# Optimization experiments

Hardware: AMD Instinct MI355X
Metric: run time of the kernel (lower is better)

Reference implementation:

```python
import jax, jax.numpy as jnp
import numpy as np

B, C_IN, N, E, C_OUT = 1, 128, 50000, 800000, 128
NEG_SLOPE = 0.3


def setup_inputs() -> dict:
    key = jax.random.key(0)
    k1, k2, k3, k4, k5 = jax.random.split(key, 5)
    in_features = jax.random.normal(k1, (B, C_IN, N), dtype=jnp.float32)
    weight = jax.random.normal(k2, (C_OUT, 2 * C_IN), dtype=jnp.float32) / np.sqrt(2 * C_IN)
    bias = jax.random.normal(k3, (C_OUT,), dtype=jnp.float32) * 0.01
    reduce_index = jax.random.randint(k4, (E,), 0, N, dtype=jnp.int64)
    gather_index = jax.random.randint(k5, (E,), 0, N, dtype=jnp.int64)
    return {"in_features": in_features, "weight": weight, "bias": bias,
            "reduce_index": reduce_index, "gather_index": gather_index}


def reference(in_features, weight, bias, reduce_index, gather_index):
    n_vertices = in_features.shape[-1]
    # gather endpoint features: [B, C, E]
    vertices = in_features[..., reduce_index]
    neighbors = in_features[..., gather_index]
    # concat [x_i, x_j - x_i] -> [B, 2C, E]
    concat = jnp.concatenate([vertices, neighbors - vertices], axis=1)
    # 1x1 Conv1d == per-edge matmul: [B, O, E]
    f_e = jnp.einsum('oc,bce->boe', weight, concat) + bias[None, :, None]
    # scatter-mean over reduce_index (include_self=False: empty segments stay 0)
    f_e_efirst = jnp.moveaxis(f_e, -1, 0)                      # [E, B, O]
    sums = jax.ops.segment_sum(f_e_efirst, reduce_index, num_segments=n_vertices)  # [N,B,O]
    counts = jax.ops.segment_sum(jnp.ones((reduce_index.shape[0],), dtype=f_e.dtype),
                                 reduce_index, num_segments=n_vertices)            # [N]
    mean = sums / jnp.maximum(counts, 1.0)[:, None, None]
    out = jnp.moveaxis(mean, 0, -1)                            # [B, O, N]
    # LeakyReLU(0.3)
    return jnp.where(out >= 0, out, NEG_SLOPE * out)
```

## Files before the change

### kernel.cpp

```cpp
#include <hip/hip_runtime.h>
#include <stddef.h>

#define CCH 128
#define CAP 64
#define FILL_CS 4096

typedef unsigned int  uint;
typedef unsigned short ushort;
typedef unsigned char uchar;
typedef short bf16x8 __attribute__((ext_vector_type(8)));
typedef float f32x4  __attribute__((ext_vector_type(4)));
typedef float f32x2  __attribute__((ext_vector_type(2)));

__device__ __forceinline__ ushort f2bf(float f) {
    uint b = __float_as_uint(f);
    b += 0x7FFFu + ((b >> 16) & 1u);
    return (ushort)(b >> 16);
}
__device__ __forceinline__ float bflo(uint u) { return __uint_as_float(u << 16); }
__device__ __forceinline__ float bfhi(uint u) { return __uint_as_float(u & 0xFFFF0000u); }

__global__ void prep_zero(const float* __restrict__ w, ushort* __restrict__ wstb,
                          int* __restrict__ zero_buf, int NZ) {
    int i = blockIdx.x * 256 + threadIdx.x;
    if (i < CCH * 256) {
        int c = i & 255;
        float v = w[i];
        if (c < 128) v -= w[i + 128];
        wstb[i] = f2bf(v);
    }
    for (int n = i; n < NZ; n += gridDim.x * 256) zero_buf[n] = 0;
}

__global__ __launch_bounds__(256) void transpose_fill(
        const float* __restrict__ x, ushort* __restrict__ xtb,
        uchar* __restrict__ xtf8,
        const int* __restrict__ ridx, const int* __restrict__ gidx,
        int* __restrict__ counts, int* __restrict__ bucket,
        int N, int E, int psz, int T, int F) {
    __shared__ float tile[CCH][33];
    int b = blockIdx.x;
    int mtf = (T < F) ? T : F;
    int twice = 2 * mtf;
    bool is_t; int sub;
    if (b < twice) { is_t = !(b & 1); sub = b >> 1; }
    else           { is_t = (T > F);  sub = (b - twice) + mtf; }
    int tid = threadIdx.x;

    if (is_t) {
        int n0 = sub * 32;
        {
            int tx = tid & 31, r = tid >> 5;
            int n = n0 + tx;
            #pragma unroll
            for (int k = 0; k < 16; ++k) {
                int c = k * 8 + r;
                tile[c][tx] = (n < N) ? x[(size_t)c * N + n] : 0.f;
            }
        }
        __syncthreads();
        #pragma unroll
        for (int p = 0; p < 2; ++p) {
            int nn = p * 16 + (tid >> 4);
            int c8 = (tid & 15) * 8;
            if (n0 + nn < N) {
                float f[8];
                #pragma unroll
                for (int j = 0; j < 8; ++j) f[j] = tile[c8 + j][nn];
                uint4 v;
                v.x = (uint)f2bf(f[0]) | ((uint)f2bf(f[1]) << 16);
                v.y = (uint)f2bf(f[2]) | ((uint)f2bf(f[3]) << 16);
                v.z = (uint)f2bf(f[4]) | ((uint)f2bf(f[5]) << 16);
                v.w = (uint)f2bf(f[6]) | ((uint)f2bf(f[7]) << 16);
                *(uint4*)(xtb + (size_t)(n0 + nn) * CCH + c8) = v;
                int p0 = __builtin_amdgcn_cvt_pk_fp8_f32(f[0], f[1], 0, false);
                p0     = __builtin_amdgcn_cvt_pk_fp8_f32(f[2], f[3], p0, true);
                int p1 = __builtin_amdgcn_cvt_pk_fp8_f32(f[4], f[5], 0, false);
                p1     = __builtin_amdgcn_cvt_pk_fp8_f32(f[6], f[7], p1, true);
                uint2 w8; w8.x = (uint)p0; w8.y = (uint)p1;
                *(uint2*)(xtf8 + (size_t)(n0 + nn) * CCH + c8) = w8;
            }
        }
    } else {
        int part  = sub & 7;
        int chunk = sub >> 3;
        int e0 = chunk * FILL_CS;
        int e1 = e0 + FILL_CS; if (e1 > E) e1 = E;
        for (int base = e0; base < e1; base += 1024) {
            int rr[4], gg[4];
            bool act[4];
            #pragma unroll
            for (int q = 0; q < 4; ++q) {
                int e = base + q * 256 + tid;
                bool in = (e < e1);
                int ec = in ? e : e0;
                rr[q] = ridx[ec];
                gg[q] = gidx[ec];
                act[q] = in && (rr[q] / psz == part);
            }
            #pragma unroll
            for (int q = 0; q < 4; ++q) {
                if (act[q]) {
                    int p = atomicAdd(&counts[rr[q]], 1);
                    if (p < CAP) bucket[rr[q] * CAP + p] = gg[q];
                }
            }
        }
    }
}

__global__ __launch_bounds__(256) void gather_mean(
        const uint*  __restrict__ xtf8u,
        const int*   __restrict__ counts,
        const int*   __restrict__ bucket,
        ushort*      __restrict__ gmb,
        int N) {
    int wave = threadIdx.x >> 6;
    int l = threadIdx.x & 63;
    int lq = l & 31;
    int half = l >> 5;
    #pragma unroll
    for (int i = 0; i < 2; ++i) {
        int n = blockIdx.x * 8 + wave * 2 + i;
        if (n >= N) return;
        int deg = __builtin_amdgcn_readfirstlane(counts[n]);
        int dg  = (deg < CAP) ? deg : CAP;
        const int* row = bucket + n * CAP;
        float4 acc = make_float4(0.f, 0.f, 0.f, 0.f);
        int k = 0;
        for (; k + 16 <= dg; k += 16) {
            uint u[8];
            #pragma unroll
            for (int q = 0; q < 8; ++q) {
                int g = row[k + 2 * q + half];
                u[q] = xtf8u[(size_t)g * 32 + lq];
            }
            #pragma unroll
            for (int q = 0; q < 8; ++q) {
                f32x2 a = __builtin_amdgcn_cvt_pk_f32_fp8(u[q], false);
                f32x2 b = __builtin_amdgcn_cvt_pk_f32_fp8(u[q], true);
                acc.x += a.x; acc.y += a.y; acc.z += b.x; acc.w += b.y;
            }
        }
        for (; k + 8 <= dg; k += 8) {
            uint u[4];
            #pragma unroll
            for (int q = 0; q < 4; ++q) {
                int g = row[k + 2 * q + half];
                u[q] = xtf8u[(size_t)g * 32 + lq];
            }
            #pragma unroll
            for (int q = 0; q < 4; ++q) {
                f32x2 a = __builtin_amdgcn_cvt_pk_f32_fp8(u[q], false);
                f32x2 b = __builtin_amdgcn_cvt_pk_f32_fp8(u[q], true);
                acc.x += a.x; acc.y += a.y; acc.z += b.x; acc.w += b.y;
            }
        }
        for (; k + 2 <= dg; k += 2) {
            int g = row[k + half];
            uint u = xtf8u[(size_t)g * 32 + lq];
            f32x2 a = __builtin_amdgcn_cvt_pk_f32_fp8(u, false);
            f32x2 b = __builtin_amdgcn_cvt_pk_f32_fp8(u, true);
            acc.x += a.x; acc.y += a.y; acc.z += b.x; acc.w += b.y;
        }
        if (k < dg && half == 0) {
            int g = row[k];
            uint u = xtf8u[(size_t)g * 32 + lq];
            f32x2 a = __builtin_amdgcn_cvt_pk_f32_fp8(u, false);
            f32x2 b = __builtin_amdgcn_cvt_pk_f32_fp8(u, true);
            acc.x += a.x; acc.y += a.y; acc.z += b.x; acc.w += b.y;
        }
        acc.x += __shfl_xor(acc.x, 32);
        acc.y += __shfl_xor(acc.y, 32);
        acc.z += __shfl_xor(acc.z, 32);
        acc.w += __shfl_xor(acc.w, 32);
        float inv = (deg > 0) ? 1.f / (float)deg : 0.f;
        if (half == 0) {
            ushort4 r;
            r.x = f2bf(acc.x * inv);
            r.y = f2bf(acc.y * inv);
            r.z = f2bf(acc.z * inv);
            r.w = f2bf(acc.w * inv);
            *(ushort4*)(gmb + (size_t)n * CCH + lq * 4) = r;
        }
    }
}

__global__ __launch_bounds__(256) void gemm_mfma(
        const ushort* __restrict__ wstb,
        const ushort* __restrict__ xtb,
        const ushort* __restrict__ gmb,
        const int*    __restrict__ counts,
        const float*  __restrict__ bias,
        float* __restrict__ out,
        int N) {
    int t = threadIdx.x;
    int wv = t >> 6;
    int l  = t & 63;
    int l15 = l & 15;
    int lk  = l >> 4;
    int n = blockIdx.x * 64 + wv * 16 + l15;
    int nc = (n < N) ? n : (N - 1);

    f32x4 acc[8];
    #pragma unroll
    for (int mf = 0; mf < 8; ++mf) acc[mf] = (f32x4){0.f, 0.f, 0.f, 0.f};

    const ushort* brow_x = xtb + (size_t)nc * CCH + lk * 8;
    const ushort* brow_g = gmb + (size_t)nc * CCH + lk * 8;
    const ushort* arow   = wstb + (size_t)l15 * 256 + lk * 8;

    #pragma unroll
    for (int ks = 0; ks < 8; ++ks) {
        const ushort* bp = (ks < 4) ? (brow_x + ks * 32) : (brow_g + (ks - 4) * 32);
        bf16x8 b = *(const bf16x8*)bp;
        #pragma unroll
        for (int mf = 0; mf < 8; ++mf) {
            bf16x8 a = *(const bf16x8*)(arow + (size_t)mf * 16 * 256 + ks * 32);
            acc[mf] = __builtin_amdgcn_mfma_f32_16x16x32_bf16(a, b, acc[mf], 0, 0, 0);
        }
    }

    if (n < N) {
        float m = (counts[n] > 0) ? 1.f : 0.f;
        #pragma unroll
        for (int mf = 0; mf < 8; ++mf) {
            #pragma unroll
            for (int r = 0; r < 4; ++r) {
                int o = mf * 16 + lk * 4 + r;
                float v = (acc[mf][r] + bias[o]) * m;
                v = (v >= 0.f) ? v : 0.3f * v;
                out[(size_t)o * N + n] = v;
            }
        }
    }
}

extern "C" void kernel_launch(void* const* d_in, const int* in_sizes, int n_in,
                              void* d_out, int out_size, void* d_ws, size_t ws_size,
                              hipStream_t stream) {
    const float* x      = (const float*)d_in[0];
    const float* weight = (const float*)d_in[1];
    const float* bias   = (const float*)d_in[2];
    const int*   ridx   = (const int*)d_in[3];
    const int*   gidx   = (const int*)d_in[4];
    float* out = (float*)d_out;

    int N = in_sizes[0] / CCH;
    int E = in_sizes[3];

    char* ws = (char*)d_ws;
    size_t xtb_bytes = (((size_t)N * CCH * sizeof(ushort)) + 63) & ~(size_t)63;
    size_t f8_bytes  = (((size_t)N * CCH * sizeof(uchar)) + 63) & ~(size_t)63;
    size_t n_bytes   = (((size_t)N * sizeof(int)) + 63) & ~(size_t)63;
    size_t bkt_bytes = (((size_t)N * CAP * sizeof(int)) + 63) & ~(size_t)63;
    size_t w_bytes   = (((size_t)CCH * 256 * sizeof(ushort)) + 63) & ~(size_t)63;

    size_t o = 0;
    ushort* xtb   = (ushort*)(ws + o); o += xtb_bytes;
    uchar*  xtf8  = (uchar*) (ws + o); o += f8_bytes;
    int*    counts= (int*)   (ws + o); o += n_bytes;
    int*    bucket= (int*)   (ws + o); o += bkt_bytes;
    ushort* wstb  = (ushort*)(ws + o); o += w_bytes;
    ushort* gmb   = (ushort*)(ws + o);

    int psz     = (N + 7) / 8;
    int nchunks = (E + FILL_CS - 1) / FILL_CS;
    int T = (N + 31) / 32;
    int F = nchunks * 8;

    prep_zero<<<128, 256, 0, stream>>>(weight, wstb, counts, N);

    transpose_fill<<<T + F, 256, 0, stream>>>(x, xtb, xtf8, ridx, gidx,
                                              counts, bucket, N, E, psz, T, F);

    gather_mean<<<(N + 7) / 8, 256, 0, stream>>>(
        (const uint*)xtf8, counts, bucket, gmb, N);

    gemm_mfma<<<(N + 63) / 64, 256, 0, stream>>>(
        wstb, xtb, gmb, counts, bias, out, N);
}
```

Before: 113.7 us.

## Store bucket indices as 16-bit and fold weight prep into transpose_fill

Neighbor indices in the per-vertex bucket are stored as ushort instead of int, halving the bucket footprint and the index traffic in both the fill and gather kernels. This is only valid while N fits in 16 bits, which holds for N=50000. The separate prep_zero kernel is removed: the weight conversion now runs in extra blocks of transpose_fill, and the counts buffer is cleared with hipMemsetAsync. That removes one kernel launch, at the cost of a memset call in its place.

```diff
diff --git a/kernel.cpp b/kernel.cpp
--- a/kernel.cpp
+++ b/kernel.cpp
@@ -20,32 +20,33 @@
 __device__ __forceinline__ float bflo(uint u) { return __uint_as_float(u << 16); }
 __device__ __forceinline__ float bfhi(uint u) { return __uint_as_float(u & 0xFFFF0000u); }
 
-__global__ void prep_zero(const float* __restrict__ w, ushort* __restrict__ wstb,
-                          int* __restrict__ zero_buf, int NZ) {
-    int i = blockIdx.x * 256 + threadIdx.x;
-    if (i < CCH * 256) {
-        int c = i & 255;
-        float v = w[i];
-        if (c < 128) v -= w[i + 128];
-        wstb[i] = f2bf(v);
-    }
-    for (int n = i; n < NZ; n += gridDim.x * 256) zero_buf[n] = 0;
-}
-
 __global__ __launch_bounds__(256) void transpose_fill(
         const float* __restrict__ x, ushort* __restrict__ xtb,
         uchar* __restrict__ xtf8,
         const int* __restrict__ ridx, const int* __restrict__ gidx,
-        int* __restrict__ counts, int* __restrict__ bucket,
+        int* __restrict__ counts, ushort* __restrict__ bucket,
+        const float* __restrict__ weight, ushort* __restrict__ wstb,
         int N, int E, int psz, int T, int F) {
     __shared__ float tile[CCH][33];
     int b = blockIdx.x;
+    int tid = threadIdx.x;
+
+    if (b >= T + F) {
+        int i = (b - (T + F)) * 256 + tid;
+        if (i < CCH * 256) {
+            int c = i & 255;
+            float v = weight[i];
+            if (c < 128) v -= weight[i + 128];
+            wstb[i] = f2bf(v);
+        }
+        return;
+    }
+
     int mtf = (T < F) ? T : F;
     int twice = 2 * mtf;
     bool is_t; int sub;
     if (b < twice) { is_t = !(b & 1); sub = b >> 1; }
     else           { is_t = (T > F);  sub = (b - twice) + mtf; }
-    int tid = threadIdx.x;
 
     if (is_t) {
         int n0 = sub * 32;
@@ -102,7 +103,7 @@
             for (int q = 0; q < 4; ++q) {
                 if (act[q]) {
                     int p = atomicAdd(&counts[rr[q]], 1);
-                    if (p < CAP) bucket[rr[q] * CAP + p] = gg[q];
+                    if (p < CAP) bucket[rr[q] * CAP + p] = (ushort)gg[q];
                 }
             }
         }
@@ -110,10 +111,10 @@
 }
 
 __global__ __launch_bounds__(256) void gather_mean(
-        const uint*  __restrict__ xtf8u,
-        const int*   __restrict__ counts,
-        const int*   __restrict__ bucket,
-        ushort*      __restrict__ gmb,
+        const uint*   __restrict__ xtf8u,
+        const int*    __restrict__ counts,
+        const ushort* __restrict__ bucket,
+        ushort*       __restrict__ gmb,
         int N) {
     int wave = threadIdx.x >> 6;
     int l = threadIdx.x & 63;
@@ -125,7 +126,7 @@
         if (n >= N) return;
         int deg = __builtin_amdgcn_readfirstlane(counts[n]);
         int dg  = (deg < CAP) ? deg : CAP;
-        const int* row = bucket + n * CAP;
+        const ushort* row = bucket + (size_t)n * CAP;
         float4 acc = make_float4(0.f, 0.f, 0.f, 0.f);
         int k = 0;
         for (; k + 16 <= dg; k += 16) {
@@ -253,14 +254,14 @@
     size_t xtb_bytes = (((size_t)N * CCH * sizeof(ushort)) + 63) & ~(size_t)63;
     size_t f8_bytes  = (((size_t)N * CCH * sizeof(uchar)) + 63) & ~(size_t)63;
     size_t n_bytes   = (((size_t)N * sizeof(int)) + 63) & ~(size_t)63;
-    size_t bkt_bytes = (((size_t)N * CAP * sizeof(int)) + 63) & ~(size_t)63;
+    size_t bkt_bytes = (((size_t)N * CAP * sizeof(ushort)) + 63) & ~(size_t)63;
     size_t w_bytes   = (((size_t)CCH * 256 * sizeof(ushort)) + 63) & ~(size_t)63;
 
     size_t o = 0;
     ushort* xtb   = (ushort*)(ws + o); o += xtb_bytes;
     uchar*  xtf8  = (uchar*) (ws + o); o += f8_bytes;
     int*    counts= (int*)   (ws + o); o += n_bytes;
-    int*    bucket= (int*)   (ws + o); o += bkt_bytes;
+    ushort* bucket= (ushort*)(ws + o); o += bkt_bytes;
     ushort* wstb  = (ushort*)(ws + o); o += w_bytes;
     ushort* gmb   = (ushort*)(ws + o);
 
@@ -268,11 +269,13 @@
     int nchunks = (E + FILL_CS - 1) / FILL_CS;
     int T = (N + 31) / 32;
     int F = nchunks * 8;
-
-    prep_zero<<<128, 256, 0, stream>>>(weight, wstb, counts, N);
-
-    transpose_fill<<<T + F, 256, 0, stream>>>(x, xtb, xtf8, ridx, gidx,
-                                              counts, bucket, N, E, psz, T, F);
+    int W = (CCH * 256 + 255) / 256;
+
+    hipMemsetAsync(counts, 0, n_bytes, stream);
+
+    transpose_fill<<<T + F + W, 256, 0, stream>>>(x, xtb, xtf8, ridx, gidx,
+                                                  counts, bucket, weight, wstb,
+                                                  N, E, psz, T, F);
 
     gather_mean<<<(N + 7) / 8, 256, 0, stream>>>(
         (const uint*)xtf8, counts, bucket, gmb, N);
```

After: 113.4 us. About the same (-0.2%).
